# Kernel tuning notes

Hardware: AMD Instinct MI355X
Metric: run time of the kernel (lower is better)

Reference implementation:

```python
import jax, jax.numpy as jnp
import numpy as np

NH, NP, HD = 8, 4, 32  # num_heads, num_points, head_dim (C=256)


def setup_inputs() -> dict:
    key = jax.random.key(0)
    k = jax.random.split(key, 8)
    B, Nq, H, W, C = 4, 8192, 128, 128, 256
    query = jax.random.normal(k[0], (B, Nq, C), jnp.float32)
    reference_points = jax.random.uniform(k[1], (B, Nq, 2), jnp.float32)
    value = jax.random.normal(k[2], (B, H * W, C), jnp.float32)
    s = 1.0 / np.sqrt(C).astype(np.float32)
    W_off = jax.random.normal(k[3], (C, NH * NP * 2), jnp.float32) * s
    b_off = jax.random.normal(k[4], (NH * NP * 2,), jnp.float32) * 0.5
    W_attn = jax.random.normal(k[5], (C, NH * NP), jnp.float32) * s
    b_attn = jnp.zeros((NH * NP,), jnp.float32)
    W_val = jax.random.normal(k[6], (C, C), jnp.float32) * s
    b_val = jnp.zeros((C,), jnp.float32)
    W_out = jax.random.normal(k[7], (C, C), jnp.float32) * s
    b_out = jnp.zeros((C,), jnp.float32)
    return dict(query=query, reference_points=reference_points, value=value,
                W_off=W_off, b_off=b_off, W_attn=W_attn, b_attn=b_attn,
                W_val=W_val, b_val=b_val, W_out=W_out, b_out=b_out, Hs=H, Ws=W)


def reference(query, reference_points, value, W_off, b_off, W_attn, b_attn,
              W_val, b_val, W_out, b_out, Hs, Ws):
    B, Nq, C = query.shape
    # sampling offsets and attention weights from queries
    off = (query @ W_off + b_off).reshape(B, Nq, NH, NP, 2)
    attn = jax.nn.softmax((query @ W_attn + b_attn).reshape(B, Nq, NH, NP), axis=-1)
    off = jnp.stack([off[..., 0] / Ws * 0.1, off[..., 1] / Hs * 0.1], axis=-1)
    loc = jnp.clip(reference_points[:, :, None, None, :] + off, 0.0, 1.0)  # [B,Nq,NH,NP,2] (x,y)
    # project value and arrange per head: [B, NH, H*W, HD]
    v = (value @ W_val + b_val).reshape(B, Hs, Ws, NH, HD)
    v = v.transpose(0, 3, 1, 2, 4).reshape(B, NH, Hs * Ws, HD)
    # grid_sample bilinear, align_corners=False, padding_mode='border':
    # pixel coord = loc*size - 0.5, clamped to [0, size-1]
    gx = jnp.clip(loc[..., 0] * Ws - 0.5, 0.0, Ws - 1.0)
    gy = jnp.clip(loc[..., 1] * Hs - 0.5, 0.0, Hs - 1.0)
    x0 = jnp.floor(gx); y0 = jnp.floor(gy)
    fx = gx - x0; fy = gy - y0
    x0i = x0.astype(jnp.int32); y0i = y0.astype(jnp.int32)
    x1i = jnp.minimum(x0i + 1, Ws - 1); y1i = jnp.minimum(y0i + 1, Hs - 1)

    def flat(xi, yi):  # [B,Nq,NH,NP] -> [B,NH,Nq*NP]
        return (yi * Ws + xi).transpose(0, 2, 1, 3).reshape(B, NH, Nq * NP)

    def gather(idx):  # -> [B,NH,Nq*NP,HD]
        return jnp.take_along_axis(v, idx[..., None], axis=2)

    def wts(w):  # [B,Nq,NH,NP] -> [B,NH,Nq*NP,1]
        return w.transpose(0, 2, 1, 3).reshape(B, NH, Nq * NP, 1)

    samp = (wts((1 - fx) * (1 - fy)) * gather(flat(x0i, y0i))
            + wts(fx * (1 - fy)) * gather(flat(x1i, y0i))
            + wts((1 - fx) * fy) * gather(flat(x0i, y1i))
            + wts(fx * fy) * gather(flat(x1i, y1i)))
    samp = samp.reshape(B, NH, Nq, NP, HD)
    aw = attn.transpose(0, 2, 1, 3)[..., None]  # [B,NH,Nq,NP,1]
    out = (samp * aw).sum(axis=3)               # [B,NH,Nq,HD]
    out = out.transpose(0, 2, 1, 3).reshape(B, Nq, C)
    return out @ W_out + b_out
```

## Files before the change

kernel.cpp:

```cpp
#include <hip/hip_runtime.h>
#include <cstddef>

#define B_   4
#define NQ_  8192
#define C_   256
#define H_   128
#define W_   128
#define HW_  (H_ * W_)
#define NH_  8
#define NP_  4
#define HD_  32

typedef __attribute__((ext_vector_type(8))) short s16x8;
typedef __attribute__((ext_vector_type(4))) float f32x4;

__device__ __forceinline__ short f2bf(float x) {
    unsigned u = __float_as_uint(x);
    unsigned r = (u + 0x7FFFu + ((u >> 16) & 1u)) >> 16;
    return (short)r;
}
__device__ __forceinline__ unsigned cvt_pk_bf16(float lo, float hi) {
    unsigned r;
    asm("v_cvt_pk_bf16_f32 %0, %1, %2" : "=v"(r) : "v"(lo), "v"(hi));
    return r;
}
__device__ __forceinline__ void gload_lds16(const void* g, void* l) {
    __builtin_amdgcn_global_load_lds(
        (const __attribute__((address_space(1))) void*)g,
        (__attribute__((address_space(3))) void*)l, 16, 0, 0);
}

__global__ void prep_kernel(const float* __restrict__ Wv, const float* __restrict__ Wo,
                            const float* __restrict__ Woff, const float* __restrict__ Wattn,
                            const float* __restrict__ boff, const float* __restrict__ battn,
                            short* __restrict__ BtVal, short* __restrict__ BtOut,
                            short* __restrict__ BtOA, float* __restrict__ biasOA)
{
    const int b = blockIdx.x, t = threadIdx.x;
    if (b < 256) {
        const int n = b;
        BtVal[(size_t)n * 256 + t] = f2bf(Wv[(size_t)t * 256 + n]);
    } else if (b < 512) {
        const int n = b - 256;
        BtOut[(size_t)n * 256 + t] = f2bf(Wo[(size_t)t * 256 + n]);
    } else {
        const int n = b - 512;
        float v = (n < 64) ? Woff[(size_t)t * 64 + n]
                           : (n < 96 ? Wattn[(size_t)t * 32 + (n - 64)] : 0.f);
        BtOA[(size_t)n * 256 + t] = f2bf(v);
        if (t == 0) biasOA[n] = (n < 64) ? boff[n] : (n < 96 ? battn[n - 64] : 0.f);
    }
}

__global__ __launch_bounds__(512, 4)
void gemm_k1k2a(const float* __restrict__ value, const short* __restrict__ BtVal,
                const float* __restrict__ b_val, short* __restrict__ vproj,
                const float* __restrict__ query, const short* __restrict__ BtOA,
                const float* __restrict__ biasOA, float* __restrict__ oa)
{
    __shared__ char  AsRaw[2 * 16384];
    __shared__ short Bs[2 * 8192];
    const int tid = threadIdx.x;
    const int l = tid & 63;
    const int w = tid >> 6;
    const int wm = w >> 2, wn = w & 3;
    const int bid = blockIdx.x;

    const float* Af;  const short* Bt;  const float* bias;
    int omode, m0;
    if (bid < 512) { Af = value; Bt = BtVal; bias = b_val;  omode = 2; m0 = bid * 128; }
    else           { Af = query; Bt = BtOA;  bias = biasOA; omode = 0; m0 = (bid - 512) * 128; }

    f32x4 acc[4][4];
#pragma unroll
    for (int i = 0; i < 4; ++i)
#pragma unroll
        for (int j = 0; j < 4; ++j) acc[i][j] = (f32x4)0.f;

    const int frag_r = l & 15;
    const int kslot  = (l >> 4) * 8;

#define STAGE_A(k0, buf)                                                      \
    _Pragma("unroll")                                                         \
    for (int r = 0; r < 2; ++r) {                                             \
        const int i = r * 512 + tid;                                          \
        const int row = i >> 3, s = i & 7;                                    \
        const int colf = (s * 4) ^ ((row & 7) << 2);          \
        gload_lds16(&Af[(size_t)(m0 + row) * 256 + (k0) + colf],              \
                    AsRaw + (buf) * 16384 + r * 8192 + w * 1024);             \
    }
#define STAGE_B(k0, buf)                                                      \
    _Pragma("unroll")                                                         \
    for (int r = 0; r < 2; ++r) {                                             \
        const int i = r * 512 + tid;                                          \
        const int row = i >> 2, cb = (i & 3) * 8;                             \
        gload_lds16(&Bt[(size_t)row * 256 + (k0) + cb],                       \
                    (char*)Bs + (buf) * 16384 + r * 8192 + w * 1024);         \
    }

    STAGE_B(0, 0);
    STAGE_A(0, 0);
    __syncthreads();

#pragma unroll
    for (int k = 0; k < 8; ++k) {
        const int cur = k & 1, nxt = cur ^ 1;
        if (k < 7) {
            STAGE_B((k + 1) * 32, nxt);
            STAGE_A((k + 1) * 32, nxt);
        }
        s16x8 a[4], b[4];
#pragma unroll
        for (int mf = 0; mf < 4; ++mf) {
            const int row = wm * 64 + mf * 16 + frag_r;
            const int g0 = (l >> 4) * 2;
            const char* base = AsRaw + cur * 16384 + row * 128;
            const float4 q0 = *(const float4*)(base + ((g0 * 16)       ^ ((row & 7) << 4)));
            const float4 q1 = *(const float4*)(base + (((g0 + 1) * 16) ^ ((row & 7) << 4)));
            union { unsigned u[4]; s16x8 v; } pk;
            pk.u[0] = cvt_pk_bf16(q0.x, q0.y);
            pk.u[1] = cvt_pk_bf16(q0.z, q0.w);
            pk.u[2] = cvt_pk_bf16(q1.x, q1.y);
            pk.u[3] = cvt_pk_bf16(q1.z, q1.w);
            a[mf] = pk.v;
        }
#pragma unroll
        for (int nf = 0; nf < 4; ++nf)
            b[nf] = *(const s16x8*)&Bs[cur * 8192 + (wn * 64 + nf * 16 + frag_r) * 32 + kslot];
#pragma unroll
        for (int mf = 0; mf < 4; ++mf)
#pragma unroll
            for (int nf = 0; nf < 4; ++nf)
                acc[mf][nf] = __builtin_amdgcn_mfma_f32_16x16x32_bf16(
                    a[mf], b[nf], acc[mf][nf], 0, 0, 0);
        if (k < 7) __syncthreads();
    }
#undef STAGE_A
#undef STAGE_B

    const int col_local = wn * 64 + (l & 15);
    const int rbase = wm * 64 + (l >> 4) * 4;
#pragma unroll
    for (int nf = 0; nf < 4; ++nf) {
        const int n = col_local + nf * 16;
        if (omode == 0 && n >= 96) continue;
        const float bs = bias[n];
#pragma unroll
        for (int mf = 0; mf < 4; ++mf) {
            const f32x4 v = acc[mf][nf];
#pragma unroll
            for (int rr = 0; rr < 4; ++rr) {
                const int m = m0 + rbase + mf * 16 + rr;
                const float o = v[rr] + bs;
                if (omode == 0) {
                    oa[(size_t)m * 128 + n] = o;
                } else {
                    const int bb = m >> 14, pix = m & (HW_ - 1);
                    const int h = n >> 5, d = n & 31;
                    vproj[((size_t)(bb * NH_ + h) * HW_ + pix) * HD_ + d] = f2bf(o);
                }
            }
        }
    }
}

__global__ __launch_bounds__(256, 4)
void gemm_k3(const short* __restrict__ A16, const short* __restrict__ Bt,
             const float* __restrict__ bias, float* __restrict__ Cp)
{
    __shared__ char  AsRaw[2 * 8192];
    __shared__ short Bs[2 * 4096];
    const int tid = threadIdx.x;
    const int l = tid & 63;
    const int w = tid >> 6;
    const int wm = w >> 1, wn = w & 1;
    const int m0 = (blockIdx.x >> 1) * 128;
    const int n0 = (blockIdx.x & 1) * 128;

    f32x4 acc[4][4];
#pragma unroll
    for (int i = 0; i < 4; ++i)
#pragma unroll
        for (int j = 0; j < 4; ++j) acc[i][j] = (f32x4)0.f;

    const int frag_r = l & 15;
    const int kslot  = (l >> 4) * 8;

#define STAGE_B3(k0, buf)                                                     \
    _Pragma("unroll")                                                         \
    for (int r = 0; r < 2; ++r) {                                             \
        const int i = r * 256 + tid;                                          \
        gload_lds16(&Bt[(size_t)(n0 + (i >> 2)) * 256 + (k0) + (i & 3) * 8],  \
                    (char*)Bs + (buf) * 8192 + r * 4096 + w * 1024);          \
    }
#define STAGE_A3(k0, buf)                                                     \
    _Pragma("unroll")                                                         \
    for (int r = 0; r < 2; ++r) {                                             \
        const int i = r * 256 + tid;                                          \
        gload_lds16(&A16[(size_t)(m0 + (i >> 2)) * 256 + (k0) + (i & 3) * 8], \
                    AsRaw + (buf) * 8192 + r * 4096 + w * 1024);              \
    }

    STAGE_B3(0, 0);
    STAGE_A3(0, 0);
    __syncthreads();

#pragma unroll
    for (int k = 0; k < 8; ++k) {
        const int cur = k & 1, nxt = cur ^ 1;
        if (k < 7) {
            STAGE_B3((k + 1) * 32, nxt);
            STAGE_A3((k + 1) * 32, nxt);
        }
        s16x8 a[4], b[4];
#pragma unroll
        for (int mf = 0; mf < 4; ++mf)
            a[mf] = *(const s16x8*)(AsRaw + cur * 8192 + (wm * 64 + mf * 16 + frag_r) * 64 + kslot * 2);
#pragma unroll
        for (int nf = 0; nf < 4; ++nf)
            b[nf] = *(const s16x8*)&Bs[cur * 4096 + (wn * 64 + nf * 16 + frag_r) * 32 + kslot];
#pragma unroll
        for (int mf = 0; mf < 4; ++mf)
#pragma unroll
            for (int nf = 0; nf < 4; ++nf)
                acc[mf][nf] = __builtin_amdgcn_mfma_f32_16x16x32_bf16(
                    a[mf], b[nf], acc[mf][nf], 0, 0, 0);
        if (k < 7) __syncthreads();
    }
#undef STAGE_A3
#undef STAGE_B3

    const int col_local = wn * 64 + (l & 15);
    const int rbase = wm * 64 + (l >> 4) * 4;
#pragma unroll
    for (int nf = 0; nf < 4; ++nf) {
        const int n = n0 + col_local + nf * 16;
        const float bs = bias[n];
#pragma unroll
        for (int mf = 0; mf < 4; ++mf) {
            const f32x4 v = acc[mf][nf];
#pragma unroll
            for (int rr = 0; rr < 4; ++rr)
                Cp[(size_t)(m0 + rbase + mf * 16 + rr) * 256 + n] = v[rr] + bs;
        }
    }
}

__global__ __launch_bounds__(256)
void sample_kernel(const float* __restrict__ oa,
                   const float* __restrict__ ref,
                   const short* __restrict__ vproj,
                   short* __restrict__ samp)
{
    __shared__ int4   s_idx[2][32];
    __shared__ float4 s_w[2][32];
    const int tid = threadIdx.x;
    const int q0 = blockIdx.x * 2;

    if (tid < 64) {
        const int qq = tid >> 5;
        const int hp = tid & 31;
        const int h = hp >> 2, p = hp & 3;
        const int q = q0 + qq;
        const float logit = oa[(size_t)q * 128 + 64 + h * 4 + p];
        float mx = fmaxf(logit, __shfl_xor(logit, 1));
        mx = fmaxf(mx, __shfl_xor(mx, 2));
        float e = __expf(logit - mx);
        float s = e + __shfl_xor(e, 1);
        s += __shfl_xor(s, 2);
        const float aw = e / s;

        const float ox = oa[(size_t)q * 128 + h * 8 + p * 2 + 0] * (0.1f / (float)W_);
        const float oy = oa[(size_t)q * 128 + h * 8 + p * 2 + 1] * (0.1f / (float)H_);
        const float lx = fminf(fmaxf(ref[(size_t)q * 2 + 0] + ox, 0.f), 1.f);
        const float ly = fminf(fmaxf(ref[(size_t)q * 2 + 1] + oy, 0.f), 1.f);
        const float gx = fminf(fmaxf(lx * (float)W_ - 0.5f, 0.f), (float)(W_ - 1));
        const float gy = fminf(fmaxf(ly * (float)H_ - 0.5f, 0.f), (float)(H_ - 1));
        const float x0f = floorf(gx), y0f = floorf(gy);
        const float fx = gx - x0f, fy = gy - y0f;
        const int x0 = (int)x0f, y0 = (int)y0f;
        const int x1 = min(x0 + 1, W_ - 1), y1 = min(y0 + 1, H_ - 1);
        s_idx[qq][hp] = make_int4((y0 * W_ + x0) * HD_, (y0 * W_ + x1) * HD_,
                                  (y1 * W_ + x0) * HD_, (y1 * W_ + x1) * HD_);
        const float gx1 = 1.f - fx, gy1 = 1.f - fy;
        s_w[qq][hp] = make_float4(aw * gx1 * gy1, aw * fx * gy1,
                                  aw * gx1 * fy,  aw * fx * fy);
    }
    __syncthreads();

    const int qq = tid >> 7;
    const int t = tid & 127;
    const int h = t >> 4;
    const int d0 = (t & 15) * 2;
    const int q = q0 + qq;
    const int b = q >> 13;
    const short* vh = vproj + (size_t)(b * NH_ + h) * (HW_ * HD_) + d0;

    float a0 = 0.f, a1 = 0.f;
#pragma unroll
    for (int p = 0; p < 4; ++p) {
        const int4   ii = s_idx[qq][h * 4 + p];
        const float4 ww = s_w[qq][h * 4 + p];
        unsigned v;
        v = *(const unsigned*)&vh[ii.x];
        a0 = fmaf(ww.x, __uint_as_float(v << 16), a0);
        a1 = fmaf(ww.x, __uint_as_float(v & 0xFFFF0000u), a1);
        v = *(const unsigned*)&vh[ii.y];
        a0 = fmaf(ww.y, __uint_as_float(v << 16), a0);
        a1 = fmaf(ww.y, __uint_as_float(v & 0xFFFF0000u), a1);
        v = *(const unsigned*)&vh[ii.z];
        a0 = fmaf(ww.z, __uint_as_float(v << 16), a0);
        a1 = fmaf(ww.z, __uint_as_float(v & 0xFFFF0000u), a1);
        v = *(const unsigned*)&vh[ii.w];
        a0 = fmaf(ww.w, __uint_as_float(v << 16), a0);
        a1 = fmaf(ww.w, __uint_as_float(v & 0xFFFF0000u), a1);
    }
    const unsigned lo = (unsigned)(unsigned short)f2bf(a0);
    const unsigned hi = (unsigned)(unsigned short)f2bf(a1);
    ((unsigned*)samp)[((size_t)q * 256 + h * HD_ + d0) >> 1] = lo | (hi << 16);
}

extern "C" void kernel_launch(void* const* d_in, const int* in_sizes, int n_in,
                              void* d_out, int out_size, void* d_ws, size_t ws_size,
                              hipStream_t stream)
{
    const float* query  = (const float*)d_in[0];
    const float* refpt  = (const float*)d_in[1];
    const float* value  = (const float*)d_in[2];
    const float* W_off  = (const float*)d_in[3];
    const float* b_off  = (const float*)d_in[4];
    const float* W_attn = (const float*)d_in[5];
    const float* b_attn = (const float*)d_in[6];
    const float* W_val  = (const float*)d_in[7];
    const float* b_val  = (const float*)d_in[8];
    const float* W_out  = (const float*)d_in[9];
    const float* b_out  = (const float*)d_in[10];
    float* out = (float*)d_out;

    char* ws = (char*)d_ws;
    short* vproj  = (short*)ws;
    short* samp   = (short*)(ws + (size_t)32 * 1024 * 1024);
    float* oa     = (float*)(ws + (size_t)48 * 1024 * 1024);
    short* BtVal  = (short*)(ws + (size_t)64 * 1024 * 1024);
    short* BtOut  = BtVal + 256 * 256;
    short* BtOA   = BtOut + 256 * 256;
    float* biasOA = (float*)(BtOA + 256 * 256);

    prep_kernel<<<768, 256, 0, stream>>>(W_val, W_out, W_off, W_attn,
                                         b_off, b_attn, BtVal, BtOut, BtOA, biasOA);

    gemm_k1k2a<<<768, 512, 0, stream>>>(value, BtVal, b_val, vproj,
                                        query, BtOA, biasOA, oa);

    sample_kernel<<<(B_ * NQ_) / 2, 256, 0, stream>>>(oa, refpt, vproj, samp);

    gemm_k3<<<512, 256, 0, stream>>>(samp, BtOut, b_out, out);
}
```

Before: 78.76 us.

## Keep full bf16 weight matrix resident in LDS and persist blocks across chunks

Replaces the 768-block input-projection GEMM with 256 larger blocks. Each block loads the whole 256x256 bf16 weight matrix into LDS once, then processes two value row-chunks and one query chunk. The A tile is loaded into registers, converted from fp32 to bf16 once, and stored into a padded LDS buffer, with explicit vmcnt waits and raw barriers to pipeline the next k-slice. This removes repeated weight staging and the per-wave fp32-to-bf16 conversion of A fragments. The cost is about 148KB of LDS per block, which limits occupancy to one block per CU and leaves fewer waves to hide latency.

Result: faster. 76.54 us (-2.8%).

```diff
diff --git a/kernel.cpp b/kernel.cpp
--- a/kernel.cpp
+++ b/kernel.cpp
@@ -29,6 +29,11 @@
         (const __attribute__((address_space(1))) void*)g,
         (__attribute__((address_space(3))) void*)l, 16, 0, 0);
 }
+
+#define SCHED0 __builtin_amdgcn_sched_barrier(0)
+#define VMW2 do { SCHED0; asm volatile("s_waitcnt vmcnt(2)" ::: "memory"); SCHED0; } while (0)
+#define VMW0 do { SCHED0; asm volatile("s_waitcnt vmcnt(0)" ::: "memory"); SCHED0; } while (0)
+#define LGKM0 do { asm volatile("s_waitcnt lgkmcnt(0)" ::: "memory"); } while (0)
 
 __global__ void prep_kernel(const float* __restrict__ Wv, const float* __restrict__ Wo,
                             const float* __restrict__ Woff, const float* __restrict__ Wattn,
@@ -52,116 +57,131 @@
     }
 }
 
-__global__ __launch_bounds__(512, 4)
-void gemm_k1k2a(const float* __restrict__ value, const short* __restrict__ BtVal,
-                const float* __restrict__ b_val, short* __restrict__ vproj,
-                const float* __restrict__ query, const short* __restrict__ BtOA,
-                const float* __restrict__ biasOA, float* __restrict__ oa)
-{
-    __shared__ char  AsRaw[2 * 16384];
-    __shared__ short Bs[2 * 8192];
+__device__ __forceinline__ void stage_B_lds(const short* __restrict__ Bt,
+                                            short* Bsm, int tid)
+{
+    const int w = tid >> 6;
+#pragma unroll
+    for (int j = 0; j < 16; ++j) {
+        const int row = j * 16 + (tid >> 5);
+        const int src = (tid & 31) ^ (row & 15);
+        gload_lds16(&Bt[(size_t)row * 256 + src * 8],
+                    (char*)Bsm + j * 8192 + w * 1024);
+    }
+}
+
+template<int OM>
+__device__ __forceinline__ void do_chunk(
+    const float* __restrict__ Af, int m0, const float* __restrict__ bias,
+    void* __restrict__ Cp, const short* Bsm, char* As80,
+    int tid, int l, int wm, int wn)
+{
+    const int arow = tid >> 2, aseg = tid & 3;
+    const int frag_r = l & 15;
+    const int g = l >> 4;
+
+    float4 pend[2][2];
+#define ISSUE(kk, slot)                                                       \
+    { const float4* p_ = (const float4*)(Af + (size_t)(m0 + arow) * 256       \
+                                         + (kk) * 32 + aseg * 8);             \
+      pend[slot][0] = p_[0]; pend[slot][1] = p_[1]; }
+#define CVTW(slot, buf)                                                       \
+    { union { unsigned u[4]; s16x8 v; } pk_;                                  \
+      pk_.u[0] = cvt_pk_bf16(pend[slot][0].x, pend[slot][0].y);               \
+      pk_.u[1] = cvt_pk_bf16(pend[slot][0].z, pend[slot][0].w);               \
+      pk_.u[2] = cvt_pk_bf16(pend[slot][1].x, pend[slot][1].y);               \
+      pk_.u[3] = cvt_pk_bf16(pend[slot][1].z, pend[slot][1].w);               \
+      *(s16x8*)(As80 + (buf) * 10240 + arow * 80 + aseg * 16) = pk_.v; }
+
+    f32x4 acc[4][4];
+#pragma unroll
+    for (int i = 0; i < 4; ++i)
+#pragma unroll
+        for (int j = 0; j < 4; ++j) acc[i][j] = (f32x4)0.f;
+
+    ISSUE(0, 0); ISSUE(1, 1); SCHED0;
+    VMW2;
+    CVTW(0, 0); LGKM0;
+    __builtin_amdgcn_s_barrier();
+
+#pragma unroll
+    for (int k = 0; k < 8; ++k) {
+        if (k <= 5) { ISSUE(k + 2, k & 1); SCHED0; }
+        s16x8 a[4], b[4];
+#pragma unroll
+        for (int mf = 0; mf < 4; ++mf) {
+            const int row = wm * 64 + mf * 16 + frag_r;
+            a[mf] = *(const s16x8*)(As80 + (k & 1) * 10240 + row * 80 + g * 16);
+        }
+#pragma unroll
+        for (int nf = 0; nf < 4; ++nf) {
+            const int brow = wn * 64 + nf * 16 + frag_r;
+            const int phys = (k * 4 + g) ^ (brow & 15);
+            b[nf] = *(const s16x8*)((const char*)Bsm + brow * 512 + phys * 16);
+        }
+#pragma unroll
+        for (int mf = 0; mf < 4; ++mf)
+#pragma unroll
+            for (int nf = 0; nf < 4; ++nf)
+                acc[mf][nf] = __builtin_amdgcn_mfma_f32_16x16x32_bf16(
+                    a[mf], b[nf], acc[mf][nf], 0, 0, 0);
+        if (k < 7) {
+            if (k <= 5) { VMW2; } else { VMW0; }
+            CVTW((k + 1) & 1, (k + 1) & 1);
+            LGKM0;
+            __builtin_amdgcn_s_barrier();
+        }
+    }
+#undef ISSUE
+#undef CVTW
+
+    const int col_local = wn * 64 + (l & 15);
+    const int rbase = wm * 64 + (l >> 4) * 4;
+#pragma unroll
+    for (int nf = 0; nf < 4; ++nf) {
+        const int n = col_local + nf * 16;
+        if (OM == 0 && n >= 96) continue;
+        const float bs = bias[n];
+#pragma unroll
+        for (int mf = 0; mf < 4; ++mf) {
+            const f32x4 v = acc[mf][nf];
+#pragma unroll
+            for (int rr = 0; rr < 4; ++rr) {
+                const int m = m0 + rbase + mf * 16 + rr;
+                const float o = v[rr] + bs;
+                if (OM == 0) {
+                    ((float*)Cp)[(size_t)m * 128 + n] = o;
+                } else {
+                    const int bb = m >> 14, pix = m & (HW_ - 1);
+                    const int h = n >> 5, d = n & 31;
+                    ((short*)Cp)[((size_t)(bb * NH_ + h) * HW_ + pix) * HD_ + d] = f2bf(o);
+                }
+            }
+        }
+    }
+}
+
+__global__ __launch_bounds__(512, 2)
+void pgemm(const float* __restrict__ value, const short* __restrict__ BtVal,
+           const float* __restrict__ b_val, short* __restrict__ vproj,
+           const float* __restrict__ query, const short* __restrict__ BtOA,
+           const float* __restrict__ biasOA, float* __restrict__ oa)
+{
+    __shared__ __align__(16) short Bsm[256 * 256];
+    __shared__ __align__(16) char  As80[2 * 10240];
     const int tid = threadIdx.x;
     const int l = tid & 63;
     const int w = tid >> 6;
     const int wm = w >> 2, wn = w & 3;
     const int bid = blockIdx.x;
 
-    const float* Af;  const short* Bt;  const float* bias;
-    int omode, m0;
-    if (bid < 512) { Af = value; Bt = BtVal; bias = b_val;  omode = 2; m0 = bid * 128; }
-    else           { Af = query; Bt = BtOA;  bias = biasOA; omode = 0; m0 = (bid - 512) * 128; }
-
-    f32x4 acc[4][4];
-#pragma unroll
-    for (int i = 0; i < 4; ++i)
-#pragma unroll
-        for (int j = 0; j < 4; ++j) acc[i][j] = (f32x4)0.f;
-
-    const int frag_r = l & 15;
-    const int kslot  = (l >> 4) * 8;
-
-#define STAGE_A(k0, buf)                                                      \
-    _Pragma("unroll")                                                         \
-    for (int r = 0; r < 2; ++r) {                                             \
-        const int i = r * 512 + tid;                                          \
-        const int row = i >> 3, s = i & 7;                                    \
-        const int colf = (s * 4) ^ ((row & 7) << 2);          \
-        gload_lds16(&Af[(size_t)(m0 + row) * 256 + (k0) + colf],              \
-                    AsRaw + (buf) * 16384 + r * 8192 + w * 1024);             \
-    }
-#define STAGE_B(k0, buf)                                                      \
-    _Pragma("unroll")                                                         \
-    for (int r = 0; r < 2; ++r) {                                             \
-        const int i = r * 512 + tid;                                          \
-        const int row = i >> 2, cb = (i & 3) * 8;                             \
-        gload_lds16(&Bt[(size_t)row * 256 + (k0) + cb],                       \
-                    (char*)Bs + (buf) * 16384 + r * 8192 + w * 1024);         \
-    }
-
-    STAGE_B(0, 0);
-    STAGE_A(0, 0);
-    __syncthreads();
-
-#pragma unroll
-    for (int k = 0; k < 8; ++k) {
-        const int cur = k & 1, nxt = cur ^ 1;
-        if (k < 7) {
-            STAGE_B((k + 1) * 32, nxt);
-            STAGE_A((k + 1) * 32, nxt);
-        }
-        s16x8 a[4], b[4];
-#pragma unroll
-        for (int mf = 0; mf < 4; ++mf) {
-            const int row = wm * 64 + mf * 16 + frag_r;
-            const int g0 = (l >> 4) * 2;
-            const char* base = AsRaw + cur * 16384 + row * 128;
-            const float4 q0 = *(const float4*)(base + ((g0 * 16)       ^ ((row & 7) << 4)));
-            const float4 q1 = *(const float4*)(base + (((g0 + 1) * 16) ^ ((row & 7) << 4)));
-            union { unsigned u[4]; s16x8 v; } pk;
-            pk.u[0] = cvt_pk_bf16(q0.x, q0.y);
-            pk.u[1] = cvt_pk_bf16(q0.z, q0.w);
-            pk.u[2] = cvt_pk_bf16(q1.x, q1.y);
-            pk.u[3] = cvt_pk_bf16(q1.z, q1.w);
-            a[mf] = pk.v;
-        }
-#pragma unroll
-        for (int nf = 0; nf < 4; ++nf)
-            b[nf] = *(const s16x8*)&Bs[cur * 8192 + (wn * 64 + nf * 16 + frag_r) * 32 + kslot];
-#pragma unroll
-        for (int mf = 0; mf < 4; ++mf)
-#pragma unroll
-            for (int nf = 0; nf < 4; ++nf)
-                acc[mf][nf] = __builtin_amdgcn_mfma_f32_16x16x32_bf16(
-                    a[mf], b[nf], acc[mf][nf], 0, 0, 0);
-        if (k < 7) __syncthreads();
-    }
-#undef STAGE_A
-#undef STAGE_B
-
-    const int col_local = wn * 64 + (l & 15);
-    const int rbase = wm * 64 + (l >> 4) * 4;
-#pragma unroll
-    for (int nf = 0; nf < 4; ++nf) {
-        const int n = col_local + nf * 16;
-        if (omode == 0 && n >= 96) continue;
-        const float bs = bias[n];
-#pragma unroll
-        for (int mf = 0; mf < 4; ++mf) {
-            const f32x4 v = acc[mf][nf];
-#pragma unroll
-            for (int rr = 0; rr < 4; ++rr) {
-                const int m = m0 + rbase + mf * 16 + rr;
-                const float o = v[rr] + bs;
-                if (omode == 0) {
-                    oa[(size_t)m * 128 + n] = o;
-                } else {
-                    const int bb = m >> 14, pix = m & (HW_ - 1);
-                    const int h = n >> 5, d = n & 31;
-                    vproj[((size_t)(bb * NH_ + h) * HW_ + pix) * HD_ + d] = f2bf(o);
-                }
-            }
-        }
-    }
+    stage_B_lds(BtVal, Bsm, tid);
+    do_chunk<2>(value, bid * 256,       b_val, vproj, Bsm, As80, tid, l, wm, wn);
+    do_chunk<2>(value, bid * 256 + 128, b_val, vproj, Bsm, As80, tid, l, wm, wn);
+
+    __builtin_amdgcn_s_barrier();
+    stage_B_lds(BtOA, Bsm, tid);
+    do_chunk<0>(query, bid * 128, biasOA, oa, Bsm, As80, tid, l, wm, wn);
 }
 
 __global__ __launch_bounds__(256, 4)
@@ -349,8 +369,8 @@
     prep_kernel<<<768, 256, 0, stream>>>(W_val, W_out, W_off, W_attn,
                                          b_off, b_attn, BtVal, BtOut, BtOA, biasOA);
 
-    gemm_k1k2a<<<768, 512, 0, stream>>>(value, BtVal, b_val, vproj,
-                                        query, BtOA, biasOA, oa);
+    pgemm<<<256, 512, 0, stream>>>(value, BtVal, b_val, vproj,
+                                   query, BtOA, biasOA, oa);
 
     sample_kernel<<<(B_ * NQ_) / 2, 256, 0, stream>>>(oa, refpt, vproj, samp);
 
```
